# Kernel optimization log

Hardware: AMD Instinct MI355X
Metric: run time of the kernel (lower is better)

Reference implementation:

```python
import jax, jax.numpy as jnp
import numpy as np


def gcn_conv(x, W, b, src, dst, n_nodes):
    """PyG GCNConv: linear transform, then symmetric-normalized sparse aggregation.
    src/dst already include self-loops. Messages flow src -> dst."""
    xw = x @ W  # [N, out]
    deg = jax.ops.segment_sum(jnp.ones_like(dst, dtype=xw.dtype), dst, num_segments=n_nodes)
    dinv = jnp.where(deg > 0, jax.lax.rsqrt(deg), 0.0)
    norm = dinv[src] * dinv[dst]  # [E]
    msg = xw[src] * norm[:, None]  # gather + scale
    out = jax.ops.segment_sum(msg, dst, num_segments=n_nodes)  # scatter-add
    return out + b


def setup_inputs() -> dict:
    key = jax.random.key(0)
    ks = jax.random.split(key, 5)
    N, E, C_in, C_out = 50000, 800000, 512, 128
    H = 2 * C_out
    x = jax.random.normal(ks[0], (N, C_in), dtype=jnp.float32)
    edge_index = jax.random.randint(ks[1], (2, E), 0, N, dtype=jnp.int64)
    def glorot(k, shape):
        lim = float(np.sqrt(6.0 / (shape[0] + shape[1])))
        return jax.random.uniform(k, shape, jnp.float32, -lim, lim)
    return {
        "x": x,
        "edge_index": edge_index,
        "W1": glorot(ks[2], (C_in, H)),
        "b1": jnp.zeros((H,), jnp.float32),
        "W_mu": glorot(ks[3], (H, C_out)),
        "b_mu": jnp.zeros((C_out,), jnp.float32),
        "W_ls": glorot(ks[4], (H, C_out)),
        "b_ls": jnp.zeros((C_out,), jnp.float32),
    }


def reference(x, edge_index, W1, b1, W_mu, b_mu, W_ls, b_ls):
    n_nodes = x.shape[0]
    # add self-loops (PyG GCNConv default add_self_loops=True)
    loops = jnp.arange(n_nodes, dtype=edge_index.dtype)
    src = jnp.concatenate([edge_index[0], loops])
    dst = jnp.concatenate([edge_index[1], loops])
    h = jax.nn.relu(gcn_conv(x, W1, b1, src, dst, n_nodes))
    mu = gcn_conv(h, W_mu, b_mu, src, dst, n_nodes)
    logstd = gcn_conv(h, W_ls, b_ls, src, dst, n_nodes)
    # stack so output is a single array [2, N, out_channels]
    return jnp.stack([mu, logstd])
```

## Files before the change

### kernel.cpp

```cpp
#include <hip/hip_runtime.h>

static inline int ceil_div(int a, int b) { return (a + b - 1) / b; }

typedef __attribute__((ext_vector_type(8))) __bf16 bf16x8;
typedef __attribute__((ext_vector_type(8))) unsigned short ushort8;
typedef __attribute__((ext_vector_type(4))) float f32x4;

#define ELLPAD 64

__device__ __forceinline__ unsigned short f2bf(float f) {
    union { float f; unsigned u; } v; v.f = f;
    unsigned r = v.u + 0x7fffu + ((v.u >> 16) & 1u);
    return (unsigned short)(r >> 16);
}
__device__ __forceinline__ float blo(unsigned u) {
    union { unsigned u; float f; } x; x.u = u << 16; return x.f;
}
__device__ __forceinline__ float bhi(unsigned u) {
    union { unsigned u; float f; } x; x.u = u & 0xffff0000u; return x.f;
}

#define SWZ(r) ((((r) & 3) ^ (((r) >> 2) & 3)))

typedef __attribute__((address_space(3))) unsigned lds_uint;
typedef __attribute__((address_space(1))) const unsigned glb_uint;
__device__ __forceinline__ void gload_lds16(const unsigned short* g, unsigned short* l) {
    __builtin_amdgcn_global_load_lds((glb_uint*)g, (lds_uint*)l, 16, 0, 0);
}

__global__ __launch_bounds__(256) void k_prep(const int* __restrict__ src, const int* __restrict__ dst,
                                              int E, int* __restrict__ cnt,
                                              unsigned short* __restrict__ ell16, int N,
                                              const float* __restrict__ x, unsigned short* __restrict__ xb,
                                              long nx,
                                              const float* __restrict__ W1, const float* __restrict__ Wmu,
                                              const float* __restrict__ Wls, unsigned short* __restrict__ W1t,
                                              unsigned short* __restrict__ Wct, int K1, int H, int Cout,
                                              int nbE, int nbX, int ilv) {
    const int b = blockIdx.x;
    int phase, idx;
    if (b < nbE + nbX) {
        if (ilv) {
            if ((b % 5) == 0 && (b / 5) < nbE) { phase = 0; idx = b / 5; }
            else { phase = 1; idx = b - min(b / 5 + 1, nbE); }
        } else {
            if (b < nbE) { phase = 0; idx = b; }
            else { phase = 1; idx = b - nbE; }
        }
    } else { phase = 2; idx = b - nbE - nbX; }

    if (phase == 0) {
        const int e = idx * 256 + threadIdx.x;
        if (e < E) {
            const int d = dst[e];
            const int r = atomicAdd(&cnt[d], 1);
            if (r < ELLPAD) ell16[(size_t)d * ELLPAD + r] = (unsigned short)src[e];
        }
    } else if (phase == 1) {
        long i = (long)idx * 2048 + (long)threadIdx.x * 8;
        if (i < nx) {
            float4 a0 = *(const float4*)(x + i);
            float4 a1 = *(const float4*)(x + i + 4);
            ushort8 t;
            t[0] = f2bf(a0.x); t[1] = f2bf(a0.y); t[2] = f2bf(a0.z); t[3] = f2bf(a0.w);
            t[4] = f2bf(a1.x); t[5] = f2bf(a1.y); t[6] = f2bf(a1.z); t[7] = f2bf(a1.w);
            *(ushort8*)(xb + i) = t;
        }
    } else {
        int t = idx * 256 + threadIdx.x;
        int n1 = H * K1;
        int n2 = 2 * Cout * H;
        if (t < n1) {
            int c = t / K1, k = t - c * K1;
            W1t[t] = f2bf(W1[(size_t)k * H + c]);
        } else if (t < n1 + n2) {
            int u = t - n1;
            int c = u / H, k = u - c * H;
            float v = (c < Cout) ? Wmu[(size_t)k * Cout + c] : Wls[(size_t)k * Cout + (c - Cout)];
            Wct[u] = f2bf(v);
        }
    }
}

__device__ __forceinline__ void gemm_tile_core(const unsigned short* __restrict__ A,
                                               const unsigned short* __restrict__ B,
                                               unsigned short* __restrict__ As, unsigned short* __restrict__ Bs,
                                               int row0, int col0, int K,
                                               int wave, int lane, f32x4 (*acc)[4]) {
    const int quad = lane >> 4, l16 = lane & 15;
    const int rw = wave & 1, cw = wave >> 1;
    const int srow = wave * 32 + (lane >> 2);
    const int slot = lane & 3;
    for (int k0 = 0; k0 < K; k0 += 32) {
#pragma unroll
        for (int t = 0; t < 2; ++t) {
            const int lr = srow + t * 16;
            const int kc = (slot ^ SWZ(lr)) * 8;
            gload_lds16(A + (size_t)(row0 + lr) * K + k0 + kc, As + (wave * 32 + t * 16) * 32);
            gload_lds16(B + (size_t)(col0 + lr) * K + k0 + kc, Bs + (wave * 32 + t * 16) * 32);
        }
        __syncthreads();
        bf16x8 af[4], bf[4];
#pragma unroll
        for (int i = 0; i < 4; ++i) {
            const int lr = rw * 64 + i * 16 + l16;
            af[i] = *(const bf16x8*)&As[lr * 32 + ((quad ^ SWZ(lr))) * 8];
            const int lc = cw * 64 + i * 16 + l16;
            bf[i] = *(const bf16x8*)&Bs[lc * 32 + ((quad ^ SWZ(lc))) * 8];
        }
#pragma unroll
        for (int i = 0; i < 4; ++i)
#pragma unroll
            for (int j = 0; j < 4; ++j)
                acc[i][j] = __builtin_amdgcn_mfma_f32_16x16x32_bf16(af[i], bf[j], acc[i][j], 0, 0, 0);
        __syncthreads();
    }
}

__global__ __launch_bounds__(256) void k_gemm1(const unsigned short* __restrict__ xb,
                                               const unsigned short* __restrict__ W1t,
                                               unsigned short* __restrict__ y, int N, int K,
                                               const int* __restrict__ cnt, float* __restrict__ dinv) {
    __shared__ __align__(16) unsigned short As[128 * 32];
    __shared__ __align__(16) unsigned short Bs[128 * 32];
    const int tid = threadIdx.x, wave = tid >> 6, lane = tid & 63;
    const int quad = lane >> 4, l16 = lane & 15;
    const int row0 = blockIdx.x * 128, col0 = blockIdx.y * 128;
    if (blockIdx.y == 0 && tid < 128) {
        const int i = row0 + tid;
        if (i < N) dinv[i] = rsqrtf((float)(cnt[i] + 1));
    }
    const int rw = wave & 1, cw = wave >> 1;
    f32x4 acc[4][4] = {};
    gemm_tile_core(xb, W1t, As, Bs, row0, col0, K, wave, lane, acc);
#pragma unroll
    for (int i = 0; i < 4; ++i) {
        const int grb = row0 + rw * 64 + i * 16 + quad * 4;
#pragma unroll
        for (int r = 0; r < 4; ++r) {
            const int row = grb + r;
            if (row < N) {
#pragma unroll
                for (int j = 0; j < 4; ++j)
                    y[(size_t)row * 256 + col0 + cw * 64 + j * 16 + l16] = f2bf(acc[i][j][r]);
            }
        }
    }
}

__global__ __launch_bounds__(256) void k_gemm2(const unsigned short* __restrict__ g,
                                               const unsigned short* __restrict__ Wct,
                                               const float* __restrict__ bmu, const float* __restrict__ bls,
                                               float* __restrict__ out, int N, int Cout) {
    __shared__ __align__(16) unsigned short As[128 * 32];
    __shared__ __align__(16) unsigned short Bs[128 * 32];
    const int K = 256;
    const int tid = threadIdx.x, wave = tid >> 6, lane = tid & 63;
    const int quad = lane >> 4, l16 = lane & 15;
    const int row0 = blockIdx.x * 128, col0 = blockIdx.y * 128;
    const int rw = wave & 1, cw = wave >> 1;
    f32x4 acc[4][4] = {};
    gemm_tile_core(g, Wct, As, Bs, row0, col0, K, wave, lane, acc);
#pragma unroll
    for (int j = 0; j < 4; ++j) {
        const int c = col0 + cw * 64 + j * 16 + l16;
        const bool is_mu = (c < Cout);
        const int ocl = is_mu ? c : (c - Cout);
        const float bv = is_mu ? bmu[ocl] : bls[ocl];
        const size_t obase = is_mu ? 0 : (size_t)N * Cout;
#pragma unroll
        for (int i = 0; i < 4; ++i) {
            const int grb = row0 + rw * 64 + i * 16 + quad * 4;
#pragma unroll
            for (int r = 0; r < 4; ++r) {
                const int row = grb + r;
                if (row < N) out[obase + (size_t)row * Cout + ocl] = acc[i][j][r] + bv;
            }
        }
    }
}

__global__ __launch_bounds__(256) void k_agg(const unsigned short* __restrict__ Yin,
                                             const unsigned short* __restrict__ ell16,
                                             const int* __restrict__ cnt,
                                             const float* __restrict__ dinv, const float* __restrict__ bias,
                                             unsigned short* __restrict__ Yout, int N, int relu_mode) {
    const int tid = threadIdx.x;
    const int wave = tid >> 6, lane = tid & 63;
    const int n = blockIdx.x * 8 + wave * 2 + (lane >> 5);
    if (n >= N) return;
    const int c = (lane & 31) * 8;
    const int L = min(cnt[n], ELLPAD);
    const unsigned short* __restrict__ nbr = ell16 + (size_t)n * ELLPAD;
    const float dn = dinv[n];
    const uint4 vn = *(const uint4*)(Yin + (size_t)n * 256 + c);
    float a0 = dn * blo(vn.x), a1 = dn * bhi(vn.x), a2 = dn * blo(vn.y), a3 = dn * bhi(vn.y);
    float a4 = dn * blo(vn.z), a5 = dn * bhi(vn.z), a6 = dn * blo(vn.w), a7 = dn * bhi(vn.w);
    int j = 0;
    for (; j + 3 < L; j += 4) {
        const ushort4 id = *(const ushort4*)(nbr + j);
        const int s0 = id.x, s1 = id.y, s2 = id.z, s3 = id.w;
        const float d0 = dinv[s0], d1 = dinv[s1], d2 = dinv[s2], d3 = dinv[s3];
        const uint4 v0 = *(const uint4*)(Yin + (size_t)s0 * 256 + c);
        const uint4 v1 = *(const uint4*)(Yin + (size_t)s1 * 256 + c);
        const uint4 v2 = *(const uint4*)(Yin + (size_t)s2 * 256 + c);
        const uint4 v3 = *(const uint4*)(Yin + (size_t)s3 * 256 + c);
        a0 = fmaf(d0, blo(v0.x), fmaf(d1, blo(v1.x), fmaf(d2, blo(v2.x), fmaf(d3, blo(v3.x), a0))));
        a1 = fmaf(d0, bhi(v0.x), fmaf(d1, bhi(v1.x), fmaf(d2, bhi(v2.x), fmaf(d3, bhi(v3.x), a1))));
        a2 = fmaf(d0, blo(v0.y), fmaf(d1, blo(v1.y), fmaf(d2, blo(v2.y), fmaf(d3, blo(v3.y), a2))));
        a3 = fmaf(d0, bhi(v0.y), fmaf(d1, bhi(v1.y), fmaf(d2, bhi(v2.y), fmaf(d3, bhi(v3.y), a3))));
        a4 = fmaf(d0, blo(v0.z), fmaf(d1, blo(v1.z), fmaf(d2, blo(v2.z), fmaf(d3, blo(v3.z), a4))));
        a5 = fmaf(d0, bhi(v0.z), fmaf(d1, bhi(v1.z), fmaf(d2, bhi(v2.z), fmaf(d3, bhi(v3.z), a5))));
        a6 = fmaf(d0, blo(v0.w), fmaf(d1, blo(v1.w), fmaf(d2, blo(v2.w), fmaf(d3, blo(v3.w), a6))));
        a7 = fmaf(d0, bhi(v0.w), fmaf(d1, bhi(v1.w), fmaf(d2, bhi(v2.w), fmaf(d3, bhi(v3.w), a7))));
    }
    for (; j < L; ++j) {
        const int s0 = nbr[j];
        const float d0 = dinv[s0];
        const uint4 v0 = *(const uint4*)(Yin + (size_t)s0 * 256 + c);
        a0 = fmaf(d0, blo(v0.x), a0); a1 = fmaf(d0, bhi(v0.x), a1);
        a2 = fmaf(d0, blo(v0.y), a2); a3 = fmaf(d0, bhi(v0.y), a3);
        a4 = fmaf(d0, blo(v0.z), a4); a5 = fmaf(d0, bhi(v0.z), a5);
        a6 = fmaf(d0, blo(v0.w), a6); a7 = fmaf(d0, bhi(v0.w), a7);
    }
    float o0, o1, o2, o3, o4, o5, o6, o7;
    if (relu_mode) {
        const float4 b0 = *(const float4*)&bias[c];
        const float4 b1 = *(const float4*)&bias[c + 4];
        o0 = fmaxf(fmaf(dn, a0, b0.x), 0.f); o1 = fmaxf(fmaf(dn, a1, b0.y), 0.f);
        o2 = fmaxf(fmaf(dn, a2, b0.z), 0.f); o3 = fmaxf(fmaf(dn, a3, b0.w), 0.f);
        o4 = fmaxf(fmaf(dn, a4, b1.x), 0.f); o5 = fmaxf(fmaf(dn, a5, b1.y), 0.f);
        o6 = fmaxf(fmaf(dn, a6, b1.z), 0.f); o7 = fmaxf(fmaf(dn, a7, b1.w), 0.f);
    } else {
        o0 = dn * a0; o1 = dn * a1; o2 = dn * a2; o3 = dn * a3;
        o4 = dn * a4; o5 = dn * a5; o6 = dn * a6; o7 = dn * a7;
    }
    uint4 o;
    o.x = (unsigned)f2bf(o0) | ((unsigned)f2bf(o1) << 16);
    o.y = (unsigned)f2bf(o2) | ((unsigned)f2bf(o3) << 16);
    o.z = (unsigned)f2bf(o4) | ((unsigned)f2bf(o5) << 16);
    o.w = (unsigned)f2bf(o6) | ((unsigned)f2bf(o7) << 16);
    *(uint4*)(Yout + (size_t)n * 256 + c) = o;
}


extern "C" void kernel_launch(void* const* d_in, const int* in_sizes, int n_in,
                              void* d_out, int out_size, void* d_ws, size_t ws_size,
                              hipStream_t stream) {
    const float* x   = (const float*)d_in[0];
    const int*   ei  = (const int*)d_in[1];
    const float* W1  = (const float*)d_in[2];
    const float* b1  = (const float*)d_in[3];
    const float* Wmu = (const float*)d_in[4];
    const float* bmu = (const float*)d_in[5];
    const float* Wls = (const float*)d_in[6];
    const float* bls = (const float*)d_in[7];

    const int H    = in_sizes[3];
    const int Cin  = in_sizes[2] / H;
    const int Cout = in_sizes[5];
    const int N    = in_sizes[0] / Cin;
    const int E    = in_sizes[1] / 2;
    const int* srcv = ei;
    const int* dstv = ei + E;

    char* w = (char*)d_ws;
    size_t off = 0;
    auto alloc = [&](size_t bytes) -> void* {
        void* p = w + off;
        off = (off + bytes + 255) & ~(size_t)255;
        return p;
    };
    int*            cnt   = (int*)alloc((size_t)N * 4);
    float*          dinv  = (float*)alloc((size_t)N * 4);
    unsigned short* ell16 = (unsigned short*)alloc((size_t)N * ELLPAD * 2);
    unsigned short* W1t   = (unsigned short*)alloc((size_t)H * Cin * 2);
    unsigned short* Wct   = (unsigned short*)alloc((size_t)2 * Cout * H * 2);
    unsigned short* xb    = (unsigned short*)alloc((size_t)N * Cin * 2);
    unsigned short* y     = (unsigned short*)alloc((size_t)N * H * 2);
    unsigned short* y2    = (unsigned short*)alloc((size_t)(N + 128) * H * 2);
    unsigned short* g     = y;
    (void)ws_size; (void)n_in; (void)out_size;

    hipMemsetAsync(cnt, 0, (size_t)N * 4, stream);

    const long nx = (long)N * Cin;
    const int nbE = ceil_div(E, 256);
    const int nbX = (int)((nx + 2047) / 2048);
    const int nbW = ceil_div(H * Cin + 2 * Cout * H, 256);
    const int ilv = (nbX == 4 * nbE) ? 1 : 0;
    k_prep<<<nbE + nbX + nbW, 256, 0, stream>>>(srcv, dstv, E, cnt, ell16, N, x, xb, nx,
                                                W1, Wmu, Wls, W1t, Wct, Cin, H, Cout, nbE, nbX, ilv);

    dim3 g1(ceil_div(N, 128), 2);
    k_gemm1<<<g1, 256, 0, stream>>>(xb, W1t, y, N, Cin, cnt, dinv);

    const int aggGrid = ceil_div(N, 8);
    k_agg<<<aggGrid, 256, 0, stream>>>(y, ell16, cnt, dinv, b1, y2, N, 1);
    k_agg<<<aggGrid, 256, 0, stream>>>(y2, ell16, cnt, dinv, nullptr, g, N, 0);

    dim3 g2(ceil_div(N, 128), 2);
    k_gemm2<<<g2, 256, 0, stream>>>(g, Wct, bmu, bls, (float*)d_out, N, Cout);
}
```

Baseline: 371.3 us.

## Split edge scatter across prep and GEMM1 kernels; compute dinv on the fly

Splits the atomic edge-to-ELL scatter into two halves. The first half is interleaved with the x-to-bf16 conversion blocks in the prep kernel, and the second half runs as extra blocks in front of the first GEMM's tiles, so the atomic work overlaps with compute-heavy blocks. The dinv buffer is removed. The aggregation kernels now recompute rsqrt(cnt+1) per neighbor from the count array, which trades a small amount of ALU work for dropping the dinv writes in GEMM1. The GEMM grid becomes a flattened 1D grid with a block-role split. Correctness still holds because cnt is final before the aggregation kernels run.

```diff
diff --git a/kernel.cpp b/kernel.cpp
--- a/kernel.cpp
+++ b/kernel.cpp
@@ -28,36 +28,30 @@
     __builtin_amdgcn_global_load_lds((glb_uint*)g, (lds_uint*)l, 16, 0, 0);
 }
 
-__global__ __launch_bounds__(256) void k_prep(const int* __restrict__ src, const int* __restrict__ dst,
-                                              int E, int* __restrict__ cnt,
-                                              unsigned short* __restrict__ ell16, int N,
+__global__ __launch_bounds__(256) void k_conv(const int* __restrict__ src, const int* __restrict__ dst,
+                                              int E1, int* __restrict__ cnt,
+                                              unsigned short* __restrict__ ell16,
                                               const float* __restrict__ x, unsigned short* __restrict__ xb,
                                               long nx,
                                               const float* __restrict__ W1, const float* __restrict__ Wmu,
                                               const float* __restrict__ Wls, unsigned short* __restrict__ W1t,
                                               unsigned short* __restrict__ Wct, int K1, int H, int Cout,
-                                              int nbE, int nbX, int ilv) {
+                                              int nbE, int nbX, int stride) {
     const int b = blockIdx.x;
-    int phase, idx;
+    const int tid = threadIdx.x;
     if (b < nbE + nbX) {
-        if (ilv) {
-            if ((b % 5) == 0 && (b / 5) < nbE) { phase = 0; idx = b / 5; }
-            else { phase = 1; idx = b - min(b / 5 + 1, nbE); }
-        } else {
-            if (b < nbE) { phase = 0; idx = b; }
-            else { phase = 1; idx = b - nbE; }
-        }
-    } else { phase = 2; idx = b - nbE - nbX; }
-
-    if (phase == 0) {
-        const int e = idx * 256 + threadIdx.x;
-        if (e < E) {
-            const int d = dst[e];
-            const int r = atomicAdd(&cnt[d], 1);
-            if (r < ELLPAD) ell16[(size_t)d * ELLPAD + r] = (unsigned short)src[e];
-        }
-    } else if (phase == 1) {
-        long i = (long)idx * 2048 + (long)threadIdx.x * 8;
+        const int q = b / stride, r = b - q * stride;
+        if (r == 0 && q < nbE) {
+            const int e = q * 256 + tid;
+            if (e < E1) {
+                const int d = dst[e];
+                const int rr = atomicAdd(&cnt[d], 1);
+                if (rr < ELLPAD) ell16[(size_t)d * ELLPAD + rr] = (unsigned short)src[e];
+            }
+            return;
+        }
+        const int scBefore = (r == 0) ? min(q, nbE) : min(q + 1, nbE);
+        const long i = (long)(b - scBefore) * 2048 + (long)tid * 8;
         if (i < nx) {
             float4 a0 = *(const float4*)(x + i);
             float4 a1 = *(const float4*)(x + i + 4);
@@ -67,7 +61,7 @@
             *(ushort8*)(xb + i) = t;
         }
     } else {
-        int t = idx * 256 + threadIdx.x;
+        int t = (b - nbE - nbX) * 256 + tid;
         int n1 = H * K1;
         int n2 = 2 * Cout * H;
         if (t < n1) {
@@ -117,19 +111,28 @@
     }
 }
 
-__global__ __launch_bounds__(256) void k_gemm1(const unsigned short* __restrict__ xb,
-                                               const unsigned short* __restrict__ W1t,
-                                               unsigned short* __restrict__ y, int N, int K,
-                                               const int* __restrict__ cnt, float* __restrict__ dinv) {
+__global__ __launch_bounds__(256) void k_gemm1s(const unsigned short* __restrict__ xb,
+                                                const unsigned short* __restrict__ W1t,
+                                                unsigned short* __restrict__ y, int N, int K,
+                                                const int* __restrict__ src, const int* __restrict__ dst,
+                                                int E0, int E, int* __restrict__ cnt,
+                                                unsigned short* __restrict__ ell16, int nbE) {
     __shared__ __align__(16) unsigned short As[128 * 32];
     __shared__ __align__(16) unsigned short Bs[128 * 32];
+    const int b = blockIdx.x;
+    if (b < nbE) {
+        const int e = E0 + b * 256 + threadIdx.x;
+        if (e < E) {
+            const int d = dst[e];
+            const int rr = atomicAdd(&cnt[d], 1);
+            if (rr < ELLPAD) ell16[(size_t)d * ELLPAD + rr] = (unsigned short)src[e];
+        }
+        return;
+    }
+    const int g = b - nbE;
+    const int row0 = (g >> 1) * 128, col0 = (g & 1) * 128;
     const int tid = threadIdx.x, wave = tid >> 6, lane = tid & 63;
     const int quad = lane >> 4, l16 = lane & 15;
-    const int row0 = blockIdx.x * 128, col0 = blockIdx.y * 128;
-    if (blockIdx.y == 0 && tid < 128) {
-        const int i = row0 + tid;
-        if (i < N) dinv[i] = rsqrtf((float)(cnt[i] + 1));
-    }
     const int rw = wave & 1, cw = wave >> 1;
     f32x4 acc[4][4] = {};
     gemm_tile_core(xb, W1t, As, Bs, row0, col0, K, wave, lane, acc);
@@ -183,16 +186,17 @@
 __global__ __launch_bounds__(256) void k_agg(const unsigned short* __restrict__ Yin,
                                              const unsigned short* __restrict__ ell16,
                                              const int* __restrict__ cnt,
-                                             const float* __restrict__ dinv, const float* __restrict__ bias,
+                                             const float* __restrict__ bias,
                                              unsigned short* __restrict__ Yout, int N, int relu_mode) {
     const int tid = threadIdx.x;
     const int wave = tid >> 6, lane = tid & 63;
     const int n = blockIdx.x * 8 + wave * 2 + (lane >> 5);
     if (n >= N) return;
     const int c = (lane & 31) * 8;
-    const int L = min(cnt[n], ELLPAD);
+    const int cn = cnt[n];
+    const int L = min(cn, ELLPAD);
     const unsigned short* __restrict__ nbr = ell16 + (size_t)n * ELLPAD;
-    const float dn = dinv[n];
+    const float dn = rsqrtf((float)(cn + 1));
     const uint4 vn = *(const uint4*)(Yin + (size_t)n * 256 + c);
     float a0 = dn * blo(vn.x), a1 = dn * bhi(vn.x), a2 = dn * blo(vn.y), a3 = dn * bhi(vn.y);
     float a4 = dn * blo(vn.z), a5 = dn * bhi(vn.z), a6 = dn * blo(vn.w), a7 = dn * bhi(vn.w);
@@ -200,7 +204,10 @@
     for (; j + 3 < L; j += 4) {
         const ushort4 id = *(const ushort4*)(nbr + j);
         const int s0 = id.x, s1 = id.y, s2 = id.z, s3 = id.w;
-        const float d0 = dinv[s0], d1 = dinv[s1], d2 = dinv[s2], d3 = dinv[s3];
+        const float d0 = rsqrtf((float)(cnt[s0] + 1));
+        const float d1 = rsqrtf((float)(cnt[s1] + 1));
+        const float d2 = rsqrtf((float)(cnt[s2] + 1));
+        const float d3 = rsqrtf((float)(cnt[s3] + 1));
         const uint4 v0 = *(const uint4*)(Yin + (size_t)s0 * 256 + c);
         const uint4 v1 = *(const uint4*)(Yin + (size_t)s1 * 256 + c);
         const uint4 v2 = *(const uint4*)(Yin + (size_t)s2 * 256 + c);
@@ -216,7 +223,7 @@
     }
     for (; j < L; ++j) {
         const int s0 = nbr[j];
-        const float d0 = dinv[s0];
+        const float d0 = rsqrtf((float)(cnt[s0] + 1));
         const uint4 v0 = *(const uint4*)(Yin + (size_t)s0 * 256 + c);
         a0 = fmaf(d0, blo(v0.x), a0); a1 = fmaf(d0, bhi(v0.x), a1);
         a2 = fmaf(d0, blo(v0.y), a2); a3 = fmaf(d0, bhi(v0.y), a3);
@@ -272,7 +279,6 @@
         return p;
     };
     int*            cnt   = (int*)alloc((size_t)N * 4);
-    float*          dinv  = (float*)alloc((size_t)N * 4);
     unsigned short* ell16 = (unsigned short*)alloc((size_t)N * ELLPAD * 2);
     unsigned short* W1t   = (unsigned short*)alloc((size_t)H * Cin * 2);
     unsigned short* Wct   = (unsigned short*)alloc((size_t)2 * Cout * H * 2);
@@ -285,19 +291,25 @@
     hipMemsetAsync(cnt, 0, (size_t)N * 4, stream);
 
     const long nx = (long)N * Cin;
-    const int nbE = ceil_div(E, 256);
-    const int nbX = (int)((nx + 2047) / 2048);
-    const int nbW = ceil_div(H * Cin + 2 * Cout * H, 256);
-    const int ilv = (nbX == 4 * nbE) ? 1 : 0;
-    k_prep<<<nbE + nbX + nbW, 256, 0, stream>>>(srcv, dstv, E, cnt, ell16, N, x, xb, nx,
-                                                W1, Wmu, Wls, W1t, Wct, Cin, H, Cout, nbE, nbX, ilv);
-
-    dim3 g1(ceil_div(N, 128), 2);
-    k_gemm1<<<g1, 256, 0, stream>>>(xb, W1t, y, N, Cin, cnt, dinv);
+    const int EA   = (E / 2) & ~255;
+    const int nbEA = ceil_div(EA, 256);
+    const int nbEB = ceil_div(E - EA, 256);
+    const int nbX  = (int)((nx + 2047) / 2048);
+    const int nbW  = ceil_div(H * Cin + 2 * Cout * H, 256);
+    int stride = (nbEA > 0) ? (nbX / nbEA + 1) : 2;
+    if (stride < 1) stride = 1;
+
+    k_conv<<<nbEA + nbX + nbW, 256, 0, stream>>>(srcv, dstv, EA, cnt, ell16, x, xb, nx,
+                                                 W1, Wmu, Wls, W1t, Wct, Cin, H, Cout,
+                                                 nbEA, nbX, stride);
+
+    const int nbG1 = ceil_div(N, 128) * 2;
+    k_gemm1s<<<nbEB + nbG1, 256, 0, stream>>>(xb, W1t, y, N, Cin,
+                                              srcv, dstv, EA, E, cnt, ell16, nbEB);
 
     const int aggGrid = ceil_div(N, 8);
-    k_agg<<<aggGrid, 256, 0, stream>>>(y, ell16, cnt, dinv, b1, y2, N, 1);
-    k_agg<<<aggGrid, 256, 0, stream>>>(y2, ell16, cnt, dinv, nullptr, g, N, 0);
+    k_agg<<<aggGrid, 256, 0, stream>>>(y, ell16, cnt, b1, y2, N, 1);
+    k_agg<<<aggGrid, 256, 0, stream>>>(y2, ell16, cnt, nullptr, g, N, 0);
 
     dim3 g2(ceil_div(N, 128), 2);
     k_gemm2<<<g2, 256, 0, stream>>>(g, Wct, bmu, bls, (float*)d_out, N, Cout);
```

Result: slower. 391.2 us (+5.4%).
